# Optimization experiments

Measured on AMD Instinct MI355X. Metric: run time of the kernel, lower is better.

## Reference

```python
import jax, jax.numpy as jnp
import numpy as np

H = 16          # num_heads
LN_EPS = 1e-5   # torch LayerNorm default


def _ln(x, g, b):
    m = jnp.mean(x, axis=-1, keepdims=True)
    v = jnp.var(x, axis=-1, keepdims=True)
    return (x - m) * jax.lax.rsqrt(v + LN_EPS) * g + b


def _cross_attn(xq, xkv, wq, wk, wv, wp, bp):
    B, N, C = xq.shape
    d = C // H
    scale = d ** -0.5
    q = (xq @ wq).reshape(B, N, H, d).transpose(0, 2, 1, 3)   # bhnd
    k = (xkv @ wk).reshape(B, N, H, d).transpose(0, 2, 1, 3)
    v = (xkv @ wv).reshape(B, N, H, d).transpose(0, 2, 1, 3)
    attn = jax.nn.softmax(jnp.einsum('bhnd,bhmd->bhnm', q, k) * scale, axis=-1)
    out = jnp.einsum('bhnm,bhmd->bhnd', attn, v).transpose(0, 2, 1, 3).reshape(B, N, C)
    return out @ wp + bp


def setup_inputs() -> dict:
    key = jax.random.key(0)
    ks = jax.random.split(key, 16)
    B, N, C, Hid = 8, 1024, 1024, 4096
    s = 0.02
    inp = {
        'x_1': jax.random.normal(ks[0], (B, N, C), jnp.float32),
        'x_2': jax.random.normal(ks[1], (B, N, C), jnp.float32),
        'x_3': jax.random.normal(ks[2], (B, N, C), jnp.float32),
        'ln11_g': jnp.ones((C,), jnp.float32), 'ln11_b': jnp.zeros((C,), jnp.float32),
        'ln12_g': jnp.ones((C,), jnp.float32), 'ln12_b': jnp.zeros((C,), jnp.float32),
        'ln21_g': jnp.ones((C,), jnp.float32), 'ln21_b': jnp.zeros((C,), jnp.float32),
        'ln23_g': jnp.ones((C,), jnp.float32), 'ln23_b': jnp.zeros((C,), jnp.float32),
        'ln2_g': jnp.ones((C,), jnp.float32), 'ln2_b': jnp.zeros((C,), jnp.float32),
        'a1_wq': s * jax.random.normal(ks[3], (C, C), jnp.float32),
        'a1_wk': s * jax.random.normal(ks[4], (C, C), jnp.float32),
        'a1_wv': s * jax.random.normal(ks[5], (C, C), jnp.float32),
        'a1_wp': s * jax.random.normal(ks[6], (C, C), jnp.float32),
        'a1_bp': jnp.zeros((C,), jnp.float32),
        'a2_wq': s * jax.random.normal(ks[7], (C, C), jnp.float32),
        'a2_wk': s * jax.random.normal(ks[8], (C, C), jnp.float32),
        'a2_wv': s * jax.random.normal(ks[9], (C, C), jnp.float32),
        'a2_wp': s * jax.random.normal(ks[10], (C, C), jnp.float32),
        'a2_bp': jnp.zeros((C,), jnp.float32),
        'fc1_w': s * jax.random.normal(ks[11], (C, Hid), jnp.float32),
        'fc1_b': jnp.zeros((Hid,), jnp.float32),
        'fc2_w': s * jax.random.normal(ks[12], (Hid, C), jnp.float32),
        'fc2_b': jnp.zeros((C,), jnp.float32),
    }
    return inp


def reference(x_1, x_2, x_3,
              ln11_g, ln11_b, ln12_g, ln12_b, ln21_g, ln21_b, ln23_g, ln23_b,
              ln2_g, ln2_b,
              a1_wq, a1_wk, a1_wv, a1_wp, a1_bp,
              a2_wq, a2_wk, a2_wv, a2_wp, a2_bp,
              fc1_w, fc1_b, fc2_w, fc2_b):
    # dual cross-attention branches + residual (drop_path/dropout are identity at p=0)
    br1 = _cross_attn(_ln(x_1, ln11_g, ln11_b), _ln(x_2, ln12_g, ln12_b),
                      a1_wq, a1_wk, a1_wv, a1_wp, a1_bp)
    br2 = _cross_attn(_ln(x_1, ln21_g, ln21_b), _ln(x_3, ln23_g, ln23_b),
                      a2_wq, a2_wk, a2_wv, a2_wp, a2_bp)
    x = x_1 + br1 + br2
    # MLP block
    h = jax.nn.gelu(_ln(x, ln2_g, ln2_b) @ fc1_w + fc1_b, approximate=False)
    x = x + (h @ fc2_w + fc2_b)
    return x
```

## Files before the change

kernel.cpp:

```cpp
#include <hip/hip_runtime.h>
#include <hip/hip_bf16.h>
#include <cstdint>

typedef unsigned short u16;
typedef __bf16 v8bf __attribute__((ext_vector_type(8)));
typedef short v4s __attribute__((ext_vector_type(4)));
typedef float v4f __attribute__((ext_vector_type(4)));

__device__ __forceinline__ u16 f2bf(float f) {
  union { float f; uint32_t u; } v; v.f = f;
  return (u16)((v.u + 0x7fffu + ((v.u >> 16) & 1u)) >> 16);
}

#define GLL16(gsrc, ldst) \
  __builtin_amdgcn_global_load_lds((__attribute__((address_space(1))) void*)(gsrc), \
      (__attribute__((address_space(3))) void*)(ldst), 16, 0, 0)

__global__ __launch_bounds__(256) void ln_kernel(
    const float* __restrict__ x, const float* __restrict__ g, const float* __restrict__ bt,
    u16* __restrict__ out)
{
  int row = blockIdx.x, tid = threadIdx.x;
  const float4* xr = (const float4*)(x + (size_t)row * 1024);
  float4 v = xr[tid];
  float s = v.x + v.y + v.z + v.w;
  float ss = v.x*v.x + v.y*v.y + v.z*v.z + v.w*v.w;
  for (int d = 1; d < 64; d <<= 1) { s += __shfl_xor(s, d); ss += __shfl_xor(ss, d); }
  __shared__ float red[8];
  int wv = tid >> 6, lane = tid & 63;
  if (lane == 0) { red[wv] = s; red[4 + wv] = ss; }
  __syncthreads();
  s  = red[0] + red[1] + red[2] + red[3];
  ss = red[4] + red[5] + red[6] + red[7];
  float mean = s * (1.f/1024.f);
  float var  = ss * (1.f/1024.f) - mean*mean;
  float rs = rsqrtf(var + 1e-5f);
  float4 gv = ((const float4*)g)[tid];
  float4 bv = ((const float4*)bt)[tid];
  ushort4 o;
  o.x = f2bf((v.x-mean)*rs*gv.x + bv.x);
  o.y = f2bf((v.y-mean)*rs*gv.y + bv.y);
  o.z = f2bf((v.z-mean)*rs*gv.z + bv.z);
  o.w = f2bf((v.w-mean)*rs*gv.w + bv.w);
  ((ushort4*)out)[(size_t)row*256 + tid] = o;
}

__global__ __launch_bounds__(256) void transpose_cast(
    const float* __restrict__ W, u16* __restrict__ WT, int K, int N)
{
  __shared__ float t[32][33];
  int tiles_n = N >> 5;
  int bn = blockIdx.x % tiles_n, bk = blockIdx.x / tiles_n;
  int tx = threadIdx.x & 31, ty = threadIdx.x >> 5;
  #pragma unroll
  for (int j = 0; j < 4; ++j)
    t[ty + j*8][tx] = W[(size_t)(bk*32 + ty + j*8) * N + bn*32 + tx];
  __syncthreads();
  #pragma unroll
  for (int j = 0; j < 4; ++j)
    WT[(size_t)(bn*32 + ty + j*8) * K + bk*32 + tx] = f2bf(t[tx][ty + j*8]);
}

template<int EPI>
__global__ __launch_bounds__(256, 2) void gemm_bf16(
    const u16* __restrict__ A, const u16* __restrict__ Bt, void* __restrict__ Cout,
    const float* __restrict__ bias, const float* __restrict__ r1, const float* __restrict__ r2,
    int M, int N, int K)
{
  int tiles_n = N >> 7;
  int bm = blockIdx.x / tiles_n, bn = blockIdx.x % tiles_n;
  int tid = threadIdx.x, wv = tid >> 6, lane = tid & 63, quad = lane >> 4, lc = lane & 15;
  int wm = wv & 1, wn = wv >> 1;

  __shared__ __align__(16) u16 lds_[16384];
  char* la = (char*)lds_;
  char* lb = (char*)lds_ + 16384;

  v4f acc[4][4] = {};

  for (int kt = 0; kt < K; kt += 64) {
    __syncthreads();
    #pragma unroll
    for (int c0 = 0; c0 < 4; ++c0) {
      int chunk = wv*4 + c0;
      int off = chunk*1024 + lane*16;
      int row = off >> 7;
      int sc  = (off >> 4) & 7;
      int lg  = sc ^ (row & 7);
      const u16* ga = A  + (size_t)(bm*128 + row) * K + kt + lg*8;
      GLL16(ga, la + chunk*1024);
      const u16* gb = Bt + (size_t)(bn*128 + row) * K + kt + lg*8;
      GLL16(gb, lb + chunk*1024);
    }
    __syncthreads();

    #pragma unroll
    for (int kc = 0; kc < 2; ++kc) {
      v8bf af[4], bfr[4];
      #pragma unroll
      for (int r = 0; r < 4; ++r) {
        int row = wm*64 + r*16 + lc;
        int sc = (kc*4 + quad) ^ (row & 7);
        af[r] = *(const v8bf*)(la + row*128 + sc*16);
      }
      #pragma unroll
      for (int c = 0; c < 4; ++c) {
        int row = wn*64 + c*16 + lc;
        int sc = (kc*4 + quad) ^ (row & 7);
        bfr[c] = *(const v8bf*)(lb + row*128 + sc*16);
      }
      #pragma unroll
      for (int r = 0; r < 4; ++r)
        #pragma unroll
        for (int c = 0; c < 4; ++c)
          acc[r][c] = __builtin_amdgcn_mfma_f32_16x16x32_bf16(af[r], bfr[c], acc[r][c], 0, 0, 0);
    }
  }

  #pragma unroll
  for (int r = 0; r < 4; ++r) {
    int grow = bm*128 + wm*64 + r*16 + quad*4;
    #pragma unroll
    for (int c = 0; c < 4; ++c) {
      int gcol = bn*128 + wn*64 + c*16 + lc;
      if (EPI == 5) {
        ushort4 o;
        o.x = f2bf(acc[r][c][0]); o.y = f2bf(acc[r][c][1]);
        o.z = f2bf(acc[r][c][2]); o.w = f2bf(acc[r][c][3]);
        *(ushort4*)((u16*)Cout + (size_t)gcol * M + grow) = o;
        continue;
      }
      float bv = (EPI != 0) ? bias[gcol] : 0.f;
      #pragma unroll
      for (int i = 0; i < 4; ++i) {
        size_t idx = (size_t)(grow + i) * N + gcol;
        float v = acc[r][c][i] + bv;
        if (EPI == 0) {
          ((u16*)Cout)[idx] = f2bf(v);
        } else if (EPI == 1) {
          float ge = 0.5f * v * (1.f + erff(v * 0.70710678118654752f));
          ((u16*)Cout)[idx] = f2bf(ge);
        } else if (EPI == 2) {
          ((float*)Cout)[idx] = v;
        } else if (EPI == 3) {
          ((float*)Cout)[idx] = v + r1[idx] + r2[idx];
        } else {
          ((float*)Cout)[idx] = v + r1[idx];
        }
      }
    }
  }
}

__global__ __launch_bounds__(256, 2) void attn_kernel(
    const u16* __restrict__ Q, const u16* __restrict__ K, const u16* __restrict__ VT,
    u16* __restrict__ O)
{
  int bid = blockIdx.x;
  int qt = bid & 15, h = (bid >> 4) & 15, b = bid >> 8;
  int tid = threadIdx.x, wv = tid >> 6, lane = tid & 63, quad = lane >> 4, lc = lane & 15;

  __shared__ __align__(16) char lds_[32768];
  char* kt_l = lds_;
  char* vt_l = lds_ + 16384;

  const float scale = 0.125f;

  v8bf qf[2];
  {
    int qrow = qt*64 + wv*16 + lc;
    const u16* qp = Q + ((size_t)(b*1024 + qrow) * 1024 + h*64 + quad*8);
    qf[0] = *(const v8bf*)qp;
    qf[1] = *(const v8bf*)(qp + 32);
  }

  float m_i = -1e30f, l_i = 0.f;
  v4f oacc[4] = {};

  for (int it = 0; it < 8; ++it) {
    int kvb = it * 128;
    __syncthreads();
    #pragma unroll
    for (int c0 = 0; c0 < 4; ++c0) {
      int ch = wv*4 + c0;
      int off = ch*1024 + lane*16;
      {
        int row = off >> 7, sc = (off >> 4) & 7, lg = sc ^ (row & 7);
        const u16* g = K + (size_t)(b*1024 + kvb + row) * 1024 + h*64 + lg*8;
        GLL16(g, kt_l + ch*1024);
      }
      {
        int row = off >> 8, sc = (off >> 4) & 15, lg = sc ^ (row & 15);
        const u16* g = VT + (size_t)(h*64 + row) * 8192 + b*1024 + kvb + lg*8;
        GLL16(g, vt_l + ch*1024);
      }
    }
    __syncthreads();

    v4f s[8] = {};
    #pragma unroll
    for (int ct = 0; ct < 8; ++ct) {
      int row = ct*16 + lc;
      #pragma unroll
      for (int kc = 0; kc < 2; ++kc) {
        int sc = (kc*4 + quad) ^ (row & 7);
        v8bf kf = *(const v8bf*)(kt_l + row*128 + sc*16);
        s[ct] = __builtin_amdgcn_mfma_f32_16x16x32_bf16(kf, qf[kc], s[ct], 0, 0, 0);
      }
    }

    float mx = m_i;
    #pragma unroll
    for (int ct = 0; ct < 8; ++ct)
      #pragma unroll
      for (int i = 0; i < 4; ++i) mx = fmaxf(mx, s[ct][i] * scale);
    mx = fmaxf(mx, __shfl_xor(mx, 16));
    mx = fmaxf(mx, __shfl_xor(mx, 32));
    float alpha = __expf(m_i - mx);
    float rs = 0.f;
    #pragma unroll
    for (int ct = 0; ct < 8; ++ct)
      #pragma unroll
      for (int i = 0; i < 4; ++i) {
        float p = __expf(s[ct][i] * scale - mx);
        s[ct][i] = p;
        rs += p;
      }
    rs += __shfl_xor(rs, 16);
    rs += __shfl_xor(rs, 32);
    l_i = l_i * alpha + rs;
    m_i = mx;
    #pragma unroll
    for (int dt = 0; dt < 4; ++dt)
      #pragma unroll
      for (int i = 0; i < 4; ++i) oacc[dt][i] *= alpha;

    #pragma unroll
    for (int ct = 0; ct < 8; ++ct) {
      v4s pfrag;
      #pragma unroll
      for (int i = 0; i < 4; ++i) pfrag[i] = (short)f2bf(s[ct][i]);
      int lg = ct*2 + (quad >> 1);
      int ho = (quad & 1) * 8;
      #pragma unroll
      for (int dt = 0; dt < 4; ++dt) {
        int rowd = dt*16 + lc;
        int sc = lg ^ (rowd & 15);
        v4s vfrag = *(const v4s*)(vt_l + rowd*256 + sc*16 + ho);
        oacc[dt] = __builtin_amdgcn_mfma_f32_16x16x16bf16_1k(vfrag, pfrag, oacc[dt], 0, 0, 0);
      }
    }
  }

  __syncthreads();
  {
    char* base = kt_l + wv*2048;
    float inv = 1.f / l_i;
    #pragma unroll
    for (int dt = 0; dt < 4; ++dt) {
      ushort4 o;
      o.x = f2bf(oacc[dt][0]*inv); o.y = f2bf(oacc[dt][1]*inv);
      o.z = f2bf(oacc[dt][2]*inv); o.w = f2bf(oacc[dt][3]*inv);
      int lg = dt*2 + (quad >> 1);
      int sc = lg ^ (lc & 7);
      *(ushort4*)(base + lc*128 + sc*16 + (quad & 1)*8) = o;
    }
  }
  __syncthreads();
  {
    char* base = kt_l + wv*2048;
    #pragma unroll
    for (int rep = 0; rep < 2; ++rep) {
      int qr = rep*8 + (lane >> 3);
      int ch = lane & 7;
      int sc = ch ^ (qr & 7);
      uint4 d = *(const uint4*)(base + qr*128 + sc*16);
      *(uint4*)(O + (size_t)(b*1024 + qt*64 + wv*16 + qr) * 1024 + h*64 + ch*8) = d;
    }
  }
}

extern "C" void kernel_launch(void* const* d_in, const int* in_sizes, int n_in,
                              void* d_out, int out_size, void* d_ws, size_t ws_size,
                              hipStream_t stream)
{
  const float* x1    = (const float*)d_in[0];
  const float* x2    = (const float*)d_in[1];
  const float* x3    = (const float*)d_in[2];
  const float* ln11g = (const float*)d_in[3];
  const float* ln11b = (const float*)d_in[4];
  const float* ln12g = (const float*)d_in[5];
  const float* ln12b = (const float*)d_in[6];
  const float* ln21g = (const float*)d_in[7];
  const float* ln21b = (const float*)d_in[8];
  const float* ln23g = (const float*)d_in[9];
  const float* ln23b = (const float*)d_in[10];
  const float* ln2g  = (const float*)d_in[11];
  const float* ln2b  = (const float*)d_in[12];
  const float* a1wq  = (const float*)d_in[13];
  const float* a1wk  = (const float*)d_in[14];
  const float* a1wv  = (const float*)d_in[15];
  const float* a1wp  = (const float*)d_in[16];
  const float* a1bp  = (const float*)d_in[17];
  const float* a2wq  = (const float*)d_in[18];
  const float* a2wk  = (const float*)d_in[19];
  const float* a2wv  = (const float*)d_in[20];
  const float* a2wp  = (const float*)d_in[21];
  const float* a2bp  = (const float*)d_in[22];
  const float* fc1w  = (const float*)d_in[23];
  const float* fc1b  = (const float*)d_in[24];
  const float* fc2w  = (const float*)d_in[25];
  const float* fc2b  = (const float*)d_in[26];

  const int M = 8192, C = 1024, HID = 4096;
  char* ws = (char*)d_ws;
  u16* WT = (u16*)ws;
  #define SLOT(i) ((void*)(ws + ((size_t)8 << 20) + (size_t)(i) * ((size_t)16 << 20)))

  dim3 blk(256);
  const int gC  = (M/128) * (C/128);
  const int gH  = (M/128) * (HID/128);
  const int tCC = (C/32) * (C/32);

  ln_kernel<<<M, blk, 0, stream>>>(x1, ln11g, ln11b, (u16*)SLOT(0));
  ln_kernel<<<M, blk, 0, stream>>>(x2, ln12g, ln12b, (u16*)SLOT(1));

  transpose_cast<<<tCC, blk, 0, stream>>>(a1wq, WT, C, C);
  gemm_bf16<0><<<gC, blk, 0, stream>>>((u16*)SLOT(0), WT, SLOT(2), nullptr, nullptr, nullptr, M, C, C);
  transpose_cast<<<tCC, blk, 0, stream>>>(a1wk, WT, C, C);
  gemm_bf16<0><<<gC, blk, 0, stream>>>((u16*)SLOT(1), WT, SLOT(3), nullptr, nullptr, nullptr, M, C, C);
  transpose_cast<<<tCC, blk, 0, stream>>>(a1wv, WT, C, C);
  gemm_bf16<5><<<gC, blk, 0, stream>>>((u16*)SLOT(1), WT, SLOT(4), nullptr, nullptr, nullptr, M, C, C);

  attn_kernel<<<2048, blk, 0, stream>>>((u16*)SLOT(2), (u16*)SLOT(3), (u16*)SLOT(4), (u16*)SLOT(0));

  transpose_cast<<<tCC, blk, 0, stream>>>(a1wp, WT, C, C);
  gemm_bf16<2><<<gC, blk, 0, stream>>>((u16*)SLOT(0), WT, SLOT(5), a1bp, nullptr, nullptr, M, C, C);

  ln_kernel<<<M, blk, 0, stream>>>(x1, ln21g, ln21b, (u16*)SLOT(1));
  ln_kernel<<<M, blk, 0, stream>>>(x3, ln23g, ln23b, (u16*)SLOT(2));

  transpose_cast<<<tCC, blk, 0, stream>>>(a2wq, WT, C, C);
  gemm_bf16<0><<<gC, blk, 0, stream>>>((u16*)SLOT(1), WT, SLOT(3), nullptr, nullptr, nullptr, M, C, C);
  transpose_cast<<<tCC, blk, 0, stream>>>(a2wk, WT, C, C);
  gemm_bf16<0><<<gC, blk, 0, stream>>>((u16*)SLOT(2), WT, SLOT(4), nullptr, nullptr, nullptr, M, C, C);
  transpose_cast<<<tCC, blk, 0, stream>>>(a2wv, WT, C, C);
  gemm_bf16<5><<<gC, blk, 0, stream>>>((u16*)SLOT(2), WT, SLOT(0), nullptr, nullptr, nullptr, M, C, C);

  attn_kernel<<<2048, blk, 0, stream>>>((u16*)SLOT(3), (u16*)SLOT(4), (u16*)SLOT(0), (u16*)SLOT(1));

  transpose_cast<<<tCC, blk, 0, stream>>>(a2wp, WT, C, C);
  gemm_bf16<3><<<gC, blk, 0, stream>>>((u16*)SLOT(1), WT, SLOT(2), a2bp, x1, (const float*)SLOT(5), M, C, C);

  ln_kernel<<<M, blk, 0, stream>>>((const float*)SLOT(2), ln2g, ln2b, (u16*)SLOT(4));
  transpose_cast<<<(C/32)*(HID/32), blk, 0, stream>>>(fc1w, WT, C, HID);
  gemm_bf16<1><<<gH, blk, 0, stream>>>((u16*)SLOT(4), WT, SLOT(5), fc1b, nullptr, nullptr, M, HID, C);
  transpose_cast<<<(HID/32)*(C/32), blk, 0, stream>>>(fc2w, WT, HID, C);
  gemm_bf16<4><<<gC, blk, 0, stream>>>((u16*)SLOT(5), WT, d_out, fc2b, (const float*)SLOT(2), nullptr, M, C, HID);
  #undef SLOT
}
```

Before: 772.1 us.

## Batch weight transposes, layernorms and QKV GEMMs into grouped launches; fuse residual-add LN

All ten weight transposes run in one launch, and the four input layernorms run in another. Q/K/V projections for each branch, and both output projections, become single grouped GEMM launches. The residual sum is fused with the MLP layernorm, and launch bounds are raised for the GEMM and attention kernels. This targets launch overhead, poor wave fill on small grids and serialized transpose/GEMM pairs. The cost is more workspace and a risk of register spills from the higher occupancy targets.

```diff
diff --git a/kernel.cpp b/kernel.cpp
--- a/kernel.cpp
+++ b/kernel.cpp
@@ -16,13 +16,49 @@
   __builtin_amdgcn_global_load_lds((__attribute__((address_space(1))) void*)(gsrc), \
       (__attribute__((address_space(3))) void*)(ldst), 16, 0, 0)
 
-__global__ __launch_bounds__(256) void ln_kernel(
-    const float* __restrict__ x, const float* __restrict__ g, const float* __restrict__ bt,
-    u16* __restrict__ out)
+struct LnBatch {
+  const float* x[4]; const float* g[4]; const float* b[4]; u16* o[4];
+};
+__global__ __launch_bounds__(256) void ln_batch_kernel(LnBatch P)
+{
+  int id = blockIdx.x >> 13;
+  int row = blockIdx.x & 8191, tid = threadIdx.x;
+  const float4* xr = (const float4*)(P.x[id] + (size_t)row * 1024);
+  float4 v = xr[tid];
+  float s = v.x + v.y + v.z + v.w;
+  float ss = v.x*v.x + v.y*v.y + v.z*v.z + v.w*v.w;
+  for (int d = 1; d < 64; d <<= 1) { s += __shfl_xor(s, d); ss += __shfl_xor(ss, d); }
+  __shared__ float red[8];
+  int wv = tid >> 6, lane = tid & 63;
+  if (lane == 0) { red[wv] = s; red[4 + wv] = ss; }
+  __syncthreads();
+  s  = red[0] + red[1] + red[2] + red[3];
+  ss = red[4] + red[5] + red[6] + red[7];
+  float mean = s * (1.f/1024.f);
+  float var  = ss * (1.f/1024.f) - mean*mean;
+  float rs = rsqrtf(var + 1e-5f);
+  float4 gv = ((const float4*)P.g[id])[tid];
+  float4 bv = ((const float4*)P.b[id])[tid];
+  ushort4 o;
+  o.x = f2bf((v.x-mean)*rs*gv.x + bv.x);
+  o.y = f2bf((v.y-mean)*rs*gv.y + bv.y);
+  o.z = f2bf((v.z-mean)*rs*gv.z + bv.z);
+  o.w = f2bf((v.w-mean)*rs*gv.w + bv.w);
+  ((ushort4*)P.o[id])[(size_t)row*256 + tid] = o;
+}
+
+__global__ __launch_bounds__(256) void addln_kernel(
+    const float* __restrict__ x1, const float* __restrict__ o1, const float* __restrict__ o2,
+    const float* __restrict__ g, const float* __restrict__ bt,
+    float* __restrict__ xsum, u16* __restrict__ out)
 {
   int row = blockIdx.x, tid = threadIdx.x;
-  const float4* xr = (const float4*)(x + (size_t)row * 1024);
-  float4 v = xr[tid];
+  size_t base = (size_t)row * 256 + tid;
+  float4 v  = ((const float4*)x1)[base];
+  float4 a  = ((const float4*)o1)[base];
+  float4 b2 = ((const float4*)o2)[base];
+  v.x += a.x + b2.x; v.y += a.y + b2.y; v.z += a.z + b2.z; v.w += a.w + b2.w;
+  ((float4*)xsum)[base] = v;
   float s = v.x + v.y + v.z + v.w;
   float ss = v.x*v.x + v.y*v.y + v.z*v.z + v.w*v.w;
   for (int d = 1; d < 64; d <<= 1) { s += __shfl_xor(s, d); ss += __shfl_xor(ss, d); }
@@ -42,15 +78,24 @@
   o.y = f2bf((v.y-mean)*rs*gv.y + bv.y);
   o.z = f2bf((v.z-mean)*rs*gv.z + bv.z);
   o.w = f2bf((v.w-mean)*rs*gv.w + bv.w);
-  ((ushort4*)out)[(size_t)row*256 + tid] = o;
-}
-
-__global__ __launch_bounds__(256) void transpose_cast(
-    const float* __restrict__ W, u16* __restrict__ WT, int K, int N)
+  ((ushort4*)out)[base] = o;
+}
+
+struct TDesc { const float* W; u16* WT; int K, N, tstart; };
+struct TBatch { TDesc d[10]; };
+__global__ __launch_bounds__(256) void transpose_batch(TBatch P)
 {
   __shared__ float t[32][33];
+  int bi = blockIdx.x;
+  int idx = 0;
+  #pragma unroll
+  for (int i = 1; i < 10; ++i) if (bi >= P.d[i].tstart) idx = i;
+  const float* W = P.d[idx].W;
+  u16* WT = P.d[idx].WT;
+  int K = P.d[idx].K, N = P.d[idx].N;
+  int loc = bi - P.d[idx].tstart;
   int tiles_n = N >> 5;
-  int bn = blockIdx.x % tiles_n, bk = blockIdx.x / tiles_n;
+  int bn = loc % tiles_n, bk = loc / tiles_n;
   int tx = threadIdx.x & 31, ty = threadIdx.x >> 5;
   #pragma unroll
   for (int j = 0; j < 4; ++j)
@@ -61,61 +106,61 @@
     WT[(size_t)(bn*32 + ty + j*8) * K + bk*32 + tx] = f2bf(t[tx][ty + j*8]);
 }
 
+#define GEMM_BODY(Aptr, Btptr, Kdim) \
+  for (int kt = 0; kt < (Kdim); kt += 64) { \
+    __syncthreads(); \
+    _Pragma("unroll") \
+    for (int c0 = 0; c0 < 4; ++c0) { \
+      int chunk = wv*4 + c0; \
+      int off = chunk*1024 + lane*16; \
+      int row = off >> 7; \
+      int sc  = (off >> 4) & 7; \
+      int lg  = sc ^ (row & 7); \
+      const u16* ga = (Aptr)  + (size_t)(bm*128 + row) * (Kdim) + kt + lg*8; \
+      GLL16(ga, la + chunk*1024); \
+      const u16* gb = (Btptr) + (size_t)(bn*128 + row) * (Kdim) + kt + lg*8; \
+      GLL16(gb, lb + chunk*1024); \
+    } \
+    __syncthreads(); \
+    _Pragma("unroll") \
+    for (int kc = 0; kc < 2; ++kc) { \
+      v8bf af[4], bfr[4]; \
+      _Pragma("unroll") \
+      for (int r = 0; r < 4; ++r) { \
+        int row = wm*64 + r*16 + lc; \
+        int sc = (kc*4 + quad) ^ (row & 7); \
+        af[r] = *(const v8bf*)(la + row*128 + sc*16); \
+      } \
+      _Pragma("unroll") \
+      for (int c = 0; c < 4; ++c) { \
+        int row = wn*64 + c*16 + lc; \
+        int sc = (kc*4 + quad) ^ (row & 7); \
+        bfr[c] = *(const v8bf*)(lb + row*128 + sc*16); \
+      } \
+      _Pragma("unroll") \
+      for (int r = 0; r < 4; ++r) \
+        _Pragma("unroll") \
+        for (int c = 0; c < 4; ++c) \
+          acc[r][c] = __builtin_amdgcn_mfma_f32_16x16x32_bf16(af[r], bfr[c], acc[r][c], 0, 0, 0); \
+    } \
+  }
+
 template<int EPI>
-__global__ __launch_bounds__(256, 2) void gemm_bf16(
+__global__ __launch_bounds__(256, 3) void gemm_bf16(
     const u16* __restrict__ A, const u16* __restrict__ Bt, void* __restrict__ Cout,
-    const float* __restrict__ bias, const float* __restrict__ r1, const float* __restrict__ r2,
+    const float* __restrict__ bias, const float* __restrict__ r1,
     int M, int N, int K)
 {
   int tiles_n = N >> 7;
   int bm = blockIdx.x / tiles_n, bn = blockIdx.x % tiles_n;
   int tid = threadIdx.x, wv = tid >> 6, lane = tid & 63, quad = lane >> 4, lc = lane & 15;
   int wm = wv & 1, wn = wv >> 1;
-
   __shared__ __align__(16) u16 lds_[16384];
   char* la = (char*)lds_;
   char* lb = (char*)lds_ + 16384;
-
   v4f acc[4][4] = {};
 
-  for (int kt = 0; kt < K; kt += 64) {
-    __syncthreads();
-    #pragma unroll
-    for (int c0 = 0; c0 < 4; ++c0) {
-      int chunk = wv*4 + c0;
-      int off = chunk*1024 + lane*16;
-      int row = off >> 7;
-      int sc  = (off >> 4) & 7;
-      int lg  = sc ^ (row & 7);
-      const u16* ga = A  + (size_t)(bm*128 + row) * K + kt + lg*8;
-      GLL16(ga, la + chunk*1024);
-      const u16* gb = Bt + (size_t)(bn*128 + row) * K + kt + lg*8;
-      GLL16(gb, lb + chunk*1024);
-    }
-    __syncthreads();
-
-    #pragma unroll
-    for (int kc = 0; kc < 2; ++kc) {
-      v8bf af[4], bfr[4];
-      #pragma unroll
-      for (int r = 0; r < 4; ++r) {
-        int row = wm*64 + r*16 + lc;
-        int sc = (kc*4 + quad) ^ (row & 7);
-        af[r] = *(const v8bf*)(la + row*128 + sc*16);
-      }
-      #pragma unroll
-      for (int c = 0; c < 4; ++c) {
-        int row = wn*64 + c*16 + lc;
-        int sc = (kc*4 + quad) ^ (row & 7);
-        bfr[c] = *(const v8bf*)(lb + row*128 + sc*16);
-      }
-      #pragma unroll
-      for (int r = 0; r < 4; ++r)
-        #pragma unroll
-        for (int c = 0; c < 4; ++c)
-          acc[r][c] = __builtin_amdgcn_mfma_f32_16x16x32_bf16(af[r], bfr[c], acc[r][c], 0, 0, 0);
-    }
-  }
+  GEMM_BODY(A, Bt, K)
 
   #pragma unroll
   for (int r = 0; r < 4; ++r) {
@@ -123,36 +168,68 @@
     #pragma unroll
     for (int c = 0; c < 4; ++c) {
       int gcol = bn*128 + wn*64 + c*16 + lc;
-      if (EPI == 5) {
+      float bv = bias[gcol];
+      #pragma unroll
+      for (int i = 0; i < 4; ++i) {
+        size_t idx = (size_t)(grow + i) * N + gcol;
+        float v = acc[r][c][i] + bv;
+        if (EPI == 1) {
+          float ge = 0.5f * v * (1.f + erff(v * 0.70710678118654752f));
+          ((u16*)Cout)[idx] = f2bf(ge);
+        } else {
+          ((float*)Cout)[idx] = v + r1[idx];
+        }
+      }
+    }
+  }
+}
+
+struct GemmDesc { const u16* A; const u16* Bt; void* C; const float* bias; int epi; };
+struct GemmBatch { GemmDesc d[3]; };
+__global__ __launch_bounds__(256, 3) void gemm_batched(GemmBatch P)
+{
+  int sub = blockIdx.x >> 9;
+  int blk = blockIdx.x & 511;
+  int bm = blk >> 3, bn = blk & 7;
+  int tid = threadIdx.x, wv = tid >> 6, lane = tid & 63, quad = lane >> 4, lc = lane & 15;
+  int wm = wv & 1, wn = wv >> 1;
+  const u16* A  = P.d[sub].A;
+  const u16* Bt = P.d[sub].Bt;
+  void* Cout    = P.d[sub].C;
+  int epi       = P.d[sub].epi;
+  __shared__ __align__(16) u16 lds_[16384];
+  char* la = (char*)lds_;
+  char* lb = (char*)lds_ + 16384;
+  v4f acc[4][4] = {};
+
+  GEMM_BODY(A, Bt, 1024)
+
+  #pragma unroll
+  for (int r = 0; r < 4; ++r) {
+    int grow = bm*128 + wm*64 + r*16 + quad*4;
+    #pragma unroll
+    for (int c = 0; c < 4; ++c) {
+      int gcol = bn*128 + wn*64 + c*16 + lc;
+      if (epi == 5) {
         ushort4 o;
         o.x = f2bf(acc[r][c][0]); o.y = f2bf(acc[r][c][1]);
         o.z = f2bf(acc[r][c][2]); o.w = f2bf(acc[r][c][3]);
-        *(ushort4*)((u16*)Cout + (size_t)gcol * M + grow) = o;
-        continue;
-      }
-      float bv = (EPI != 0) ? bias[gcol] : 0.f;
-      #pragma unroll
-      for (int i = 0; i < 4; ++i) {
-        size_t idx = (size_t)(grow + i) * N + gcol;
-        float v = acc[r][c][i] + bv;
-        if (EPI == 0) {
-          ((u16*)Cout)[idx] = f2bf(v);
-        } else if (EPI == 1) {
-          float ge = 0.5f * v * (1.f + erff(v * 0.70710678118654752f));
-          ((u16*)Cout)[idx] = f2bf(ge);
-        } else if (EPI == 2) {
-          ((float*)Cout)[idx] = v;
-        } else if (EPI == 3) {
-          ((float*)Cout)[idx] = v + r1[idx] + r2[idx];
-        } else {
-          ((float*)Cout)[idx] = v + r1[idx];
-        }
-      }
-    }
-  }
-}
-
-__global__ __launch_bounds__(256, 2) void attn_kernel(
+        *(ushort4*)((u16*)Cout + (size_t)gcol * 8192 + grow) = o;
+      } else if (epi == 0) {
+        #pragma unroll
+        for (int i = 0; i < 4; ++i)
+          ((u16*)Cout)[(size_t)(grow + i) * 1024 + gcol] = f2bf(acc[r][c][i]);
+      } else {
+        float bv = P.d[sub].bias[gcol];
+        #pragma unroll
+        for (int i = 0; i < 4; ++i)
+          ((float*)Cout)[(size_t)(grow + i) * 1024 + gcol] = acc[r][c][i] + bv;
+      }
+    }
+  }
+}
+
+__global__ __launch_bounds__(256, 4) void attn_kernel(
     const u16* __restrict__ Q, const u16* __restrict__ K, const u16* __restrict__ VT,
     u16* __restrict__ O)
 {
@@ -312,50 +389,70 @@
   const float* fc2w  = (const float*)d_in[25];
   const float* fc2b  = (const float*)d_in[26];
 
-  const int M = 8192, C = 1024, HID = 4096;
   char* ws = (char*)d_ws;
-  u16* WT = (u16*)ws;
-  #define SLOT(i) ((void*)(ws + ((size_t)8 << 20) + (size_t)(i) * ((size_t)16 << 20)))
+  const size_t MB = (size_t)1 << 20;
+  u16* wtq1 = (u16*)(ws + 0*MB);  u16* wtk1 = (u16*)(ws + 2*MB);
+  u16* wtv1 = (u16*)(ws + 4*MB);  u16* wtp1 = (u16*)(ws + 6*MB);
+  u16* wtq2 = (u16*)(ws + 8*MB);  u16* wtk2 = (u16*)(ws + 10*MB);
+  u16* wtv2 = (u16*)(ws + 12*MB); u16* wtp2 = (u16*)(ws + 14*MB);
+  u16* wtf1 = (u16*)(ws + 16*MB); u16* wtf2 = (u16*)(ws + 24*MB);
+  u16* xq1   = (u16*)(ws + 32*MB);  u16* xkv1 = (u16*)(ws + 48*MB);
+  u16* xq2   = (u16*)(ws + 64*MB);  u16* xkv2 = (u16*)(ws + 80*MB);
+  u16* Qb    = (u16*)(ws + 96*MB);  u16* Kb   = (u16*)(ws + 112*MB);
+  u16* VTb   = (u16*)(ws + 128*MB);
+  u16* O1    = (u16*)(ws + 32*MB);
+  u16* O2    = (u16*)(ws + 48*MB);
+  float* o1f = (float*)(ws + 64*MB);
+  float* o2f = (float*)(ws + 96*MB);
+  u16* ln2o  = (u16*)(ws + 32*MB);
+  u16* hbuf  = (u16*)(ws + 48*MB);
 
   dim3 blk(256);
-  const int gC  = (M/128) * (C/128);
-  const int gH  = (M/128) * (HID/128);
-  const int tCC = (C/32) * (C/32);
-
-  ln_kernel<<<M, blk, 0, stream>>>(x1, ln11g, ln11b, (u16*)SLOT(0));
-  ln_kernel<<<M, blk, 0, stream>>>(x2, ln12g, ln12b, (u16*)SLOT(1));
-
-  transpose_cast<<<tCC, blk, 0, stream>>>(a1wq, WT, C, C);
-  gemm_bf16<0><<<gC, blk, 0, stream>>>((u16*)SLOT(0), WT, SLOT(2), nullptr, nullptr, nullptr, M, C, C);
-  transpose_cast<<<tCC, blk, 0, stream>>>(a1wk, WT, C, C);
-  gemm_bf16<0><<<gC, blk, 0, stream>>>((u16*)SLOT(1), WT, SLOT(3), nullptr, nullptr, nullptr, M, C, C);
-  transpose_cast<<<tCC, blk, 0, stream>>>(a1wv, WT, C, C);
-  gemm_bf16<5><<<gC, blk, 0, stream>>>((u16*)SLOT(1), WT, SLOT(4), nullptr, nullptr, nullptr, M, C, C);
-
-  attn_kernel<<<2048, blk, 0, stream>>>((u16*)SLOT(2), (u16*)SLOT(3), (u16*)SLOT(4), (u16*)SLOT(0));
-
-  transpose_cast<<<tCC, blk, 0, stream>>>(a1wp, WT, C, C);
-  gemm_bf16<2><<<gC, blk, 0, stream>>>((u16*)SLOT(0), WT, SLOT(5), a1bp, nullptr, nullptr, M, C, C);
-
-  ln_kernel<<<M, blk, 0, stream>>>(x1, ln21g, ln21b, (u16*)SLOT(1));
-  ln_kernel<<<M, blk, 0, stream>>>(x3, ln23g, ln23b, (u16*)SLOT(2));
-
-  transpose_cast<<<tCC, blk, 0, stream>>>(a2wq, WT, C, C);
-  gemm_bf16<0><<<gC, blk, 0, stream>>>((u16*)SLOT(1), WT, SLOT(3), nullptr, nullptr, nullptr, M, C, C);
-  transpose_cast<<<tCC, blk, 0, stream>>>(a2wk, WT, C, C);
-  gemm_bf16<0><<<gC, blk, 0, stream>>>((u16*)SLOT(2), WT, SLOT(4), nullptr, nullptr, nullptr, M, C, C);
-  transpose_cast<<<tCC, blk, 0, stream>>>(a2wv, WT, C, C);
-  gemm_bf16<5><<<gC, blk, 0, stream>>>((u16*)SLOT(2), WT, SLOT(0), nullptr, nullptr, nullptr, M, C, C);
-
-  attn_kernel<<<2048, blk, 0, stream>>>((u16*)SLOT(3), (u16*)SLOT(4), (u16*)SLOT(0), (u16*)SLOT(1));
-
-  transpose_cast<<<tCC, blk, 0, stream>>>(a2wp, WT, C, C);
-  gemm_bf16<3><<<gC, blk, 0, stream>>>((u16*)SLOT(1), WT, SLOT(2), a2bp, x1, (const float*)SLOT(5), M, C, C);
-
-  ln_kernel<<<M, blk, 0, stream>>>((const float*)SLOT(2), ln2g, ln2b, (u16*)SLOT(4));
-  transpose_cast<<<(C/32)*(HID/32), blk, 0, stream>>>(fc1w, WT, C, HID);
-  gemm_bf16<1><<<gH, blk, 0, stream>>>((u16*)SLOT(4), WT, SLOT(5), fc1b, nullptr, nullptr, M, HID, C);
-  transpose_cast<<<(HID/32)*(C/32), blk, 0, stream>>>(fc2w, WT, HID, C);
-  gemm_bf16<4><<<gC, blk, 0, stream>>>((u16*)SLOT(5), WT, d_out, fc2b, (const float*)SLOT(2), nullptr, M, C, HID);
-  #undef SLOT
-}
+
+  TBatch tb;
+  const float* Ws[10]  = {a1wq, a1wk, a1wv, a1wp, a2wq, a2wk, a2wv, a2wp, fc1w, fc2w};
+  u16* WTs[10]         = {wtq1, wtk1, wtv1, wtp1, wtq2, wtk2, wtv2, wtp2, wtf1, wtf2};
+  int Kd[10] = {1024,1024,1024,1024,1024,1024,1024,1024,1024,4096};
+  int Nd[10] = {1024,1024,1024,1024,1024,1024,1024,1024,4096,1024};
+  int ts = 0;
+  for (int i = 0; i < 10; ++i) {
+    tb.d[i] = {Ws[i], WTs[i], Kd[i], Nd[i], ts};
+    ts += (Kd[i]/32) * (Nd[i]/32);
+  }
+  transpose_batch<<<ts, blk, 0, stream>>>(tb);
+
+  LnBatch lb;
+  lb.x[0]=x1; lb.g[0]=ln11g; lb.b[0]=ln11b; lb.o[0]=xq1;
+  lb.x[1]=x2; lb.g[1]=ln12g; lb.b[1]=ln12b; lb.o[1]=xkv1;
+  lb.x[2]=x1; lb.g[2]=ln21g; lb.b[2]=ln21b; lb.o[2]=xq2;
+  lb.x[3]=x3; lb.g[3]=ln23g; lb.b[3]=ln23b; lb.o[3]=xkv2;
+  ln_batch_kernel<<<4*8192, blk, 0, stream>>>(lb);
+
+  GemmBatch g1;
+  g1.d[0] = {xq1,  wtq1, Qb,  nullptr, 0};
+  g1.d[1] = {xkv1, wtk1, Kb,  nullptr, 0};
+  g1.d[2] = {xkv1, wtv1, VTb, nullptr, 5};
+  gemm_batched<<<1536, blk, 0, stream>>>(g1);
+
+  attn_kernel<<<2048, blk, 0, stream>>>(Qb, Kb, VTb, O1);
+
+  GemmBatch g2;
+  g2.d[0] = {xq2,  wtq2, Qb,  nullptr, 0};
+  g2.d[1] = {xkv2, wtk2, Kb,  nullptr, 0};
+  g2.d[2] = {xkv2, wtv2, VTb, nullptr, 5};
+  gemm_batched<<<1536, blk, 0, stream>>>(g2);
+
+  attn_kernel<<<2048, blk, 0, stream>>>(Qb, Kb, VTb, O2);
+
+  GemmBatch gp;
+  gp.d[0] = {O1, wtp1, o1f, a1bp, 2};
+  gp.d[1] = {O2, wtp2, o2f, a2bp, 2};
+  gp.d[2] = gp.d[0];
+  gemm_batched<<<1024, blk, 0, stream>>>(gp);
+
+  addln_kernel<<<8192, blk, 0, stream>>>(x1, o1f, o2f, ln2g, ln2b, (float*)d_out, ln2o);
+
+  gemm_bf16<1><<<(8192/128)*(4096/128), blk, 0, stream>>>(ln2o, wtf1, hbuf, fc1b, nullptr, 8192, 4096, 1024);
+
+  gemm_bf16<4><<<(8192/128)*(1024/128), blk, 0, stream>>>(hbuf, wtf2, d_out, fc2b, (const float*)d_out, 8192, 1024, 4096);
+}
```

New measurement: 783.4 us. About the same (+1.5%).
